# Performance work log

Hardware: AMD Instinct MI355X
Metric: run time of the kernel (lower is better)

The kernel has to match this reference:

```python
import jax, jax.numpy as jnp
import numpy as np

RADIUS = 4
NUM_LEVELS = 4
STRIDES = (1, 1, 1, 1)


def _level_corr(f1, f2, coords, r, stride):
    """Windowed bilinear correlation at one pyramid level.
    f1: [B,C,H,W] (full-res features), f2: [B,C,H2,W2] (level features),
    coords: [B,2,H,W] (x,y) already scaled to f2's resolution.
    Returns [B,(2r+1)^2,H,W].
    """
    B, C, H, W = f1.shape
    H2, W2 = f2.shape[2], f2.shape[3]
    f1t = jnp.transpose(f1, (0, 2, 3, 1))                     # [B,H,W,C]
    f2f = jnp.transpose(f2, (0, 2, 3, 1)).reshape(B, H2 * W2, C)
    d = jnp.arange(-r, r + 1, dtype=f1.dtype) * stride
    dy, dx = jnp.meshgrid(d, d, indexing='ij')
    deltas = jnp.stack([dx.ravel(), dy.ravel()], axis=-1)      # [(2r+1)^2, 2]

    def one_offset(delta):
        x = coords[:, 0] + delta[0]                            # [B,H,W]
        y = coords[:, 1] + delta[1]
        x0 = jnp.floor(x)
        y0 = jnp.floor(y)
        acc = jnp.zeros((B, H, W), f1.dtype)
        # 4 bilinear corners, zero padding outside the feature map
        for cx in (0.0, 1.0):
            for cy in (0.0, 1.0):
                xc = x0 + cx
                yc = y0 + cy
                w = (1.0 - jnp.abs(x - xc)) * (1.0 - jnp.abs(y - yc))
                valid = (xc >= 0) & (xc <= W2 - 1) & (yc >= 0) & (yc <= H2 - 1)
                idx = (jnp.clip(yc, 0, H2 - 1) * W2 + jnp.clip(xc, 0, W2 - 1)).astype(jnp.int32)
                g = jax.vmap(lambda t, i: t[i])(f2f, idx.reshape(B, -1)).reshape(B, H, W, C)
                acc = acc + jnp.where(valid, w, 0.0) * jnp.einsum('bhwc,bhwc->bhw', f1t, g)
        return acc                                             # [B,H,W]

    corr = jax.lax.map(one_offset, deltas)                     # [K,B,H,W]
    return jnp.transpose(corr, (1, 0, 2, 3))                   # [B,K,H,W]


def _corr_block(fmap1, fmap2s, coords):
    C = fmap1.shape[1]
    outs = []
    for i, f2 in enumerate(fmap2s):
        outs.append(_level_corr(fmap1, f2, coords / (2.0 ** i), RADIUS, STRIDES[i]))
    corr = jnp.concatenate(outs, axis=1)                       # [B, L*(2r+1)^2, H, W]
    return corr / jnp.sqrt(jnp.asarray(C, fmap1.dtype))


def setup_inputs() -> dict:
    key = jax.random.key(0)
    ks = jax.random.split(key, 6)
    B, C, H, W = 2, 256, 64, 64
    inp = {'fmap1': jax.random.normal(ks[0], (B, C, H, W), jnp.float32)}
    for i in range(NUM_LEVELS):
        h, w = H >> i, W >> i
        inp['fmap2_%d' % i] = jax.random.normal(ks[1 + i], (B, C, h, w), jnp.float32)
    gy, gx = jnp.meshgrid(jnp.arange(H, dtype=jnp.float32), jnp.arange(W, dtype=jnp.float32), indexing='ij')
    base = jnp.broadcast_to(jnp.stack([gx, gy], 0)[None], (B, 2, H, W))
    flow = 2.0 * jax.random.normal(jax.random.fold_in(key, 99), (B, 2, H, W), jnp.float32)
    inp['coords'] = base + flow
    return inp


def reference(fmap1, fmap2_0, fmap2_1, fmap2_2, fmap2_3, coords):
    return _corr_block(fmap1, [fmap2_0, fmap2_1, fmap2_2, fmap2_3], coords)
```

## Files before the change

### kernel.cpp

```cpp
#include <hip/hip_runtime.h>

#define RADIUS 4
#define KK 81
#define HWP 4096

typedef _Float16 f16x8 __attribute__((ext_vector_type(8)));
typedef _Float16 f16x4 __attribute__((ext_vector_type(4)));
typedef float    f32x4 __attribute__((ext_vector_type(4)));

#define OFF_F1T  0u
#define OFF_L0   4194304u
#define OFF_L1   8388608u
#define OFF_L2   9437184u
#define OFF_L3   9699328u
#define OFF_ZPAD 9764864u
#define OFF_END  9765376u

__global__ __launch_bounds__(256) void stage_kernel(
    const float* __restrict__ f1, const float* __restrict__ l0,
    const float* __restrict__ l1, const float* __restrict__ l2,
    const float* __restrict__ l3, char* __restrict__ wsB)
{
    __shared__ float tile[32][36];
    const int bx = blockIdx.x;
    const int b  = blockIdx.z;
    const int r0 = blockIdx.y * 32;
    const int t  = threadIdx.x;
    if (bx == 0 && blockIdx.y == 0 && b == 0 && t < 128)
        ((float*)(wsB + OFF_ZPAD))[t] = 0.0f;
    const float* src; _Float16* dst; int S, s0i;
    if (bx < 128)      { src = f1; dst = (_Float16*)(wsB + OFF_F1T); S = 4096; s0i = bx; }
    else if (bx < 256) { src = l0; dst = (_Float16*)(wsB + OFF_L0);  S = 4096; s0i = bx - 128; }
    else if (bx < 288) { src = l1; dst = (_Float16*)(wsB + OFF_L1);  S = 1024; s0i = bx - 256; }
    else if (bx < 296) { src = l2; dst = (_Float16*)(wsB + OFF_L2);  S = 256;  s0i = bx - 288; }
    else               { src = l3; dst = (_Float16*)(wsB + OFF_L3);  S = 64;   s0i = bx - 296; }
    const int s0 = s0i * 32;
    src += (size_t)b * 256 * S;
    dst += (size_t)b * S * 256;
    {
        const int row = t >> 3, cg = t & 7;
        *(f32x4*)&tile[row][cg * 4] =
            *(const f32x4*)&src[(size_t)(r0 + row) * S + s0 + cg * 4];
    }
    __syncthreads();
    {
        const int sidx = t >> 3, chg = t & 7;
        f16x4 o;
        o[0] = (_Float16)tile[chg * 4 + 0][sidx];
        o[1] = (_Float16)tile[chg * 4 + 1][sidx];
        o[2] = (_Float16)tile[chg * 4 + 2][sidx];
        o[3] = (_Float16)tile[chg * 4 + 3][sidx];
        *(f16x4*)&dst[(size_t)(s0 + sidx) * 256 + r0 + chg * 4] = o;
    }
}

__global__ __launch_bounds__(256, 2) void corr_mfma_kernel(
    const char* __restrict__ wsB,
    const float* __restrict__ coords,
    float* __restrict__ out)
{
    __shared__ float sD[32][104];
    __shared__ int   sIx[32], sIy[32];
    __shared__ float sW[32][4];
    __shared__ int   sBox[5];

    const int bx   = blockIdx.x;
    const int lvl  = blockIdx.y;
    const int tile = ((bx & 7) << 5) | (bx >> 3);
    const int b    = tile >> 7;
    const int t7   = tile & 127;
    const int tr4  = (t7 >> 3) << 2;
    const int tc8  = (t7 & 7) << 3;
    const int t    = threadIdx.x;
    const int l    = t & 63;
    const int wid  = t >> 6;

    const int sh = 6 - lvl;
    const int W2 = 1 << sh;

    for (int i = t; i < 32 * 104; i += 256)
        ((float*)sD)[i] = 0.0f;

    if (t < 32) {
        const int hwc = ((tr4 + (t >> 3)) << 6) + tc8 + (t & 7);
        const float sc = 1.0f / (float)(1 << lvl);
        const float xs = coords[((size_t)b * 2 + 0) * HWP + hwc] * sc;
        const float ys = coords[((size_t)b * 2 + 1) * HWP + hwc] * sc;
        const float x0f = floorf(xs), y0f = floorf(ys);
        sIx[t] = (int)x0f; sIy[t] = (int)y0f;
        const float fx = xs - x0f, fy = ys - y0f;
        sW[t][0] = (1.f - fx) * (1.f - fy);
        sW[t][1] = fx * (1.f - fy);
        sW[t][2] = (1.f - fx) * fy;
        sW[t][3] = fx * fy;
    }
    __syncthreads();
    if (t == 0) {
        int rlo = 1 << 20, rhi = -(1 << 20), clo = 1 << 20, chi = -(1 << 20);
        for (int px = 0; px < 32; ++px) {
            rlo = min(rlo, sIy[px]); rhi = max(rhi, sIy[px]);
            clo = min(clo, sIx[px]); chi = max(chi, sIx[px]);
        }
        const int rl = max(rlo - RADIUS, 0);
        const int rh = min(rhi + RADIUS + 1, W2 - 1);
        const int cf = max(clo - RADIUS, 0);
        const int ce = min(chi + RADIUS + 1, W2 - 1);
        const int nr = rh - rl + 1;
        const int nt = (ce >= cf) ? ((ce - cf + 16) >> 4) : 0;
        sBox[0] = rl;
        sBox[1] = cf;
        sBox[2] = nt;
        sBox[3] = (nr > 0) ? nr * nt : 0;
        sBox[4] = 65535 / max(nt, 1) + 1;
    }

    const int hwA0 = ((tr4 + ((l & 15) >> 3)) << 6) + tc8 + (l & 7);
    const int hwA1 = ((tr4 + 2 + ((l & 15) >> 3)) << 6) + tc8 + (l & 7);
    const char* ap0 = wsB + OFF_F1T + ((size_t)(b * HWP + hwA0)) * 512 + ((l >> 4) << 4);
    const char* ap1 = wsB + OFF_F1T + ((size_t)(b * HWP + hwA1)) * 512 + ((l >> 4) << 4);
    const f16x8 a00 = __builtin_bit_cast(f16x8, *(const f32x4*)(ap0));
    const f16x8 a01 = __builtin_bit_cast(f16x8, *(const f32x4*)(ap0 + 64));
    const f16x8 a02 = __builtin_bit_cast(f16x8, *(const f32x4*)(ap0 + 128));
    const f16x8 a03 = __builtin_bit_cast(f16x8, *(const f32x4*)(ap0 + 192));
    const f16x8 a04 = __builtin_bit_cast(f16x8, *(const f32x4*)(ap0 + 256));
    const f16x8 a05 = __builtin_bit_cast(f16x8, *(const f32x4*)(ap0 + 320));
    const f16x8 a06 = __builtin_bit_cast(f16x8, *(const f32x4*)(ap0 + 384));
    const f16x8 a07 = __builtin_bit_cast(f16x8, *(const f32x4*)(ap0 + 448));
    const f16x8 a10 = __builtin_bit_cast(f16x8, *(const f32x4*)(ap1));
    const f16x8 a11 = __builtin_bit_cast(f16x8, *(const f32x4*)(ap1 + 64));
    const f16x8 a12 = __builtin_bit_cast(f16x8, *(const f32x4*)(ap1 + 128));
    const f16x8 a13 = __builtin_bit_cast(f16x8, *(const f32x4*)(ap1 + 192));
    const f16x8 a14 = __builtin_bit_cast(f16x8, *(const f32x4*)(ap1 + 256));
    const f16x8 a15 = __builtin_bit_cast(f16x8, *(const f32x4*)(ap1 + 320));
    const f16x8 a16 = __builtin_bit_cast(f16x8, *(const f32x4*)(ap1 + 384));
    const f16x8 a17 = __builtin_bit_cast(f16x8, *(const f32x4*)(ap1 + 448));
    __syncthreads();

    const int rlo = sBox[0], cfi = sBox[1], ntw = sBox[2];
    const int ntot = sBox[3], inv = sBox[4];
    const unsigned lvbase = ((lvl == 0) ? OFF_L0 : (lvl == 1) ? OFF_L1
                           : (lvl == 2) ? OFF_L2 : OFF_L3)
                          + (((unsigned)b << (2 * sh)) << 9);
    const int coff = l & 15;
    const int ksub = (l >> 4) << 4;
    const unsigned zp = OFF_ZPAD + (unsigned)ksub;

    const int pg0 = (l >> 4) << 2;
    const int pg1 = 16 + pg0;
    const int iy0 = sIy[pg0 + 0], ix0 = sIx[pg0 + 0];
    const int iy1 = sIy[pg0 + 1], ix1 = sIx[pg0 + 1];
    const int iy2 = sIy[pg0 + 2], ix2 = sIx[pg0 + 2];
    const int iy3 = sIy[pg0 + 3], ix3 = sIx[pg0 + 3];
    const int iy4 = sIy[pg1 + 0], ix4 = sIx[pg1 + 0];
    const int iy5 = sIy[pg1 + 1], ix5 = sIx[pg1 + 1];
    const int iy6 = sIy[pg1 + 2], ix6 = sIx[pg1 + 2];
    const int iy7 = sIy[pg1 + 3], ix7 = sIx[pg1 + 3];

    asm volatile("s_waitcnt vmcnt(0)" ::: "memory");
    __builtin_amdgcn_sched_barrier(0);

#define DECODE(U_, RR_, JJ_) { const unsigned q__ = ((unsigned)((U_) * inv)) >> 16; \
        JJ_ = (U_) - (int)q__ * ntw; RR_ = rlo + (int)q__; }

#define ISSUE(R_, J_, B0, B1, B2, B3, B4, B5, B6, B7) { \
        const int col_ = cfi + ((J_) << 4) + coff; \
        const bool ok_ = (unsigned)col_ < (unsigned)W2; \
        const unsigned cb_ = ok_ ? (lvbase + ((unsigned)(((R_) << sh) + col_) << 9) + (unsigned)ksub) : zp; \
        const char* gp_ = wsB + cb_; \
        asm volatile("global_load_dwordx4 %0, %1, off"            : "=v"(B0) : "v"(gp_)); \
        asm volatile("global_load_dwordx4 %0, %1, off offset:64"  : "=v"(B1) : "v"(gp_)); \
        asm volatile("global_load_dwordx4 %0, %1, off offset:128" : "=v"(B2) : "v"(gp_)); \
        asm volatile("global_load_dwordx4 %0, %1, off offset:192" : "=v"(B3) : "v"(gp_)); \
        asm volatile("global_load_dwordx4 %0, %1, off offset:256" : "=v"(B4) : "v"(gp_)); \
        asm volatile("global_load_dwordx4 %0, %1, off offset:320" : "=v"(B5) : "v"(gp_)); \
        asm volatile("global_load_dwordx4 %0, %1, off offset:384" : "=v"(B6) : "v"(gp_)); \
        asm volatile("global_load_dwordx4 %0, %1, off offset:448" : "=v"(B7) : "v"(gp_)); }

#define WAITV8 { asm volatile("s_waitcnt vmcnt(8)" ::: "memory"); __builtin_amdgcn_sched_barrier(0); }
#define WAITV0 { asm volatile("s_waitcnt vmcnt(0)" ::: "memory"); __builtin_amdgcn_sched_barrier(0); }

#define CONSUMET(R_, J_, B0, B1, B2, B3, B4, B5, B6, B7) { \
        f32x4 ac00 = {0.f,0.f,0.f,0.f}, ac01 = {0.f,0.f,0.f,0.f}; \
        f32x4 ac10 = {0.f,0.f,0.f,0.f}, ac11 = {0.f,0.f,0.f,0.f}; \
        ac00 = __builtin_amdgcn_mfma_f32_16x16x32_f16(a00, __builtin_bit_cast(f16x8, B0), ac00, 0, 0, 0); \
        ac10 = __builtin_amdgcn_mfma_f32_16x16x32_f16(a10, __builtin_bit_cast(f16x8, B0), ac10, 0, 0, 0); \
        ac01 = __builtin_amdgcn_mfma_f32_16x16x32_f16(a01, __builtin_bit_cast(f16x8, B1), ac01, 0, 0, 0); \
        ac11 = __builtin_amdgcn_mfma_f32_16x16x32_f16(a11, __builtin_bit_cast(f16x8, B1), ac11, 0, 0, 0); \
        ac00 = __builtin_amdgcn_mfma_f32_16x16x32_f16(a02, __builtin_bit_cast(f16x8, B2), ac00, 0, 0, 0); \
        ac10 = __builtin_amdgcn_mfma_f32_16x16x32_f16(a12, __builtin_bit_cast(f16x8, B2), ac10, 0, 0, 0); \
        ac01 = __builtin_amdgcn_mfma_f32_16x16x32_f16(a03, __builtin_bit_cast(f16x8, B3), ac01, 0, 0, 0); \
        ac11 = __builtin_amdgcn_mfma_f32_16x16x32_f16(a13, __builtin_bit_cast(f16x8, B3), ac11, 0, 0, 0); \
        ac00 = __builtin_amdgcn_mfma_f32_16x16x32_f16(a04, __builtin_bit_cast(f16x8, B4), ac00, 0, 0, 0); \
        ac10 = __builtin_amdgcn_mfma_f32_16x16x32_f16(a14, __builtin_bit_cast(f16x8, B4), ac10, 0, 0, 0); \
        ac01 = __builtin_amdgcn_mfma_f32_16x16x32_f16(a05, __builtin_bit_cast(f16x8, B5), ac01, 0, 0, 0); \
        ac11 = __builtin_amdgcn_mfma_f32_16x16x32_f16(a15, __builtin_bit_cast(f16x8, B5), ac11, 0, 0, 0); \
        ac00 = __builtin_amdgcn_mfma_f32_16x16x32_f16(a06, __builtin_bit_cast(f16x8, B6), ac00, 0, 0, 0); \
        ac10 = __builtin_amdgcn_mfma_f32_16x16x32_f16(a16, __builtin_bit_cast(f16x8, B6), ac10, 0, 0, 0); \
        ac01 = __builtin_amdgcn_mfma_f32_16x16x32_f16(a07, __builtin_bit_cast(f16x8, B7), ac01, 0, 0, 0); \
        ac11 = __builtin_amdgcn_mfma_f32_16x16x32_f16(a17, __builtin_bit_cast(f16x8, B7), ac11, 0, 0, 0); \
        const f32x4 s0 = ac00 + ac01; \
        const f32x4 s1 = ac10 + ac11; \
        const int col_ = cfi + ((J_) << 4) + coff; \
        const int p0 = (R_) - iy0 + RADIUS, q0 = col_ - ix0 + RADIUS; \
        if ((unsigned)p0 < 10u && (unsigned)q0 < 10u) sD[pg0 + 0][p0 * 10 + q0] = s0[0]; \
        const int p1 = (R_) - iy1 + RADIUS, q1 = col_ - ix1 + RADIUS; \
        if ((unsigned)p1 < 10u && (unsigned)q1 < 10u) sD[pg0 + 1][p1 * 10 + q1] = s0[1]; \
        const int p2 = (R_) - iy2 + RADIUS, q2 = col_ - ix2 + RADIUS; \
        if ((unsigned)p2 < 10u && (unsigned)q2 < 10u) sD[pg0 + 2][p2 * 10 + q2] = s0[2]; \
        const int p3 = (R_) - iy3 + RADIUS, q3 = col_ - ix3 + RADIUS; \
        if ((unsigned)p3 < 10u && (unsigned)q3 < 10u) sD[pg0 + 3][p3 * 10 + q3] = s0[3]; \
        const int p4 = (R_) - iy4 + RADIUS, q4 = col_ - ix4 + RADIUS; \
        if ((unsigned)p4 < 10u && (unsigned)q4 < 10u) sD[pg1 + 0][p4 * 10 + q4] = s1[0]; \
        const int p5 = (R_) - iy5 + RADIUS, q5 = col_ - ix5 + RADIUS; \
        if ((unsigned)p5 < 10u && (unsigned)q5 < 10u) sD[pg1 + 1][p5 * 10 + q5] = s1[1]; \
        const int p6 = (R_) - iy6 + RADIUS, q6 = col_ - ix6 + RADIUS; \
        if ((unsigned)p6 < 10u && (unsigned)q6 < 10u) sD[pg1 + 2][p6 * 10 + q6] = s1[2]; \
        const int p7 = (R_) - iy7 + RADIUS, q7 = col_ - ix7 + RADIUS; \
        if ((unsigned)p7 < 10u && (unsigned)q7 < 10u) sD[pg1 + 3][p7 * 10 + q7] = s1[3]; }

    {
        f32x4 X0, X1, X2, X3, X4, X5, X6, X7;
        f32x4 Y0, Y1, Y2, Y3, Y4, Y5, Y6, Y7;
        int ua = wid;
        if (ua < ntot) {
            int ra, ja, rb, jb;
            DECODE(ua, ra, ja);
            ISSUE(ra, ja, X0, X1, X2, X3, X4, X5, X6, X7);
            int ub = ua + 4;
            for (;;) {
                const bool bv = (ub < ntot);
                if (bv) { DECODE(ub, rb, jb); ISSUE(rb, jb, Y0, Y1, Y2, Y3, Y4, Y5, Y6, Y7); WAITV8; }
                else    { WAITV0; }
                CONSUMET(ra, ja, X0, X1, X2, X3, X4, X5, X6, X7);
                if (!bv) break;
                ua = ub + 4;
                const bool av = (ua < ntot);
                if (av) { DECODE(ua, ra, ja); ISSUE(ra, ja, X0, X1, X2, X3, X4, X5, X6, X7); WAITV8; }
                else    { WAITV0; }
                CONSUMET(rb, jb, Y0, Y1, Y2, Y3, Y4, Y5, Y6, Y7);
                if (!av) break;
                ub = ua + 4;
            }
        }
    }
#undef DECODE
#undef ISSUE
#undef WAITV8
#undef WAITV0
#undef CONSUMET
    __syncthreads();

    for (int j = t; j < 32 * KK; j += 256) {
        const int px = j & 31;
        const int k  = j >> 5;
        const int p  = (k * 57) >> 9;
        const int q  = k - p * 9;
        const int bi = p * 10 + q;
        const float* dd = sD[px];
        const float v = (sW[px][0] * dd[bi]      + sW[px][1] * dd[bi + 1] +
                         sW[px][2] * dd[bi + 10] + sW[px][3] * dd[bi + 11]) * 0.0625f;
        const int hwp = ((tr4 + (px >> 3)) << 6) + tc8 + (px & 7);
        out[((size_t)b * 324 + lvl * KK + k) * HWP + hwp] = v;
    }
}

__global__ __launch_bounds__(128) void corr_level_kernel(
    const float* __restrict__ f1, const float* __restrict__ f2,
    const float* __restrict__ coords, float* __restrict__ out,
    int H2, int W2, float scale, int lvl)
{
    __shared__ float sf1[256];
    __shared__ float sDl[100];
    const int pix = blockIdx.x;
    const int b   = pix >> 12;
    const int hw  = pix & 4095;
    const int t   = threadIdx.x;
    for (int c = t; c < 256; c += 128)
        sf1[c] = f1[((size_t)b * 256 + c) * 4096 + hw];
    __syncthreads();
    const float xs = coords[((size_t)b * 2 + 0) * 4096 + hw] * scale;
    const float ys = coords[((size_t)b * 2 + 1) * 4096 + hw] * scale;
    const float x0f = floorf(xs), y0f = floorf(ys);
    const float fx = xs - x0f, fy = ys - y0f;
    const int ix0 = (int)x0f, iy0 = (int)y0f;
    if (t < 100) {
        const int p = t / 10, q = t - p * 10;
        const int row = iy0 - 4 + p, col = ix0 - 4 + q;
        float acc = 0.0f;
        if (row >= 0 && row < H2 && col >= 0 && col < W2) {
            const size_t step = (size_t)H2 * W2;
            const size_t base = (size_t)b * 256 * step + (size_t)row * W2 + col;
            #pragma unroll 4
            for (int c = 0; c < 256; ++c)
                acc += f2[base + (size_t)c * step] * sf1[c];
        }
        sDl[t] = acc;
    }
    __syncthreads();
    if (t < 81) {
        const int p = t / 9, q = t - p * 9;
        const float d00 = sDl[p * 10 + q];
        const float d01 = sDl[p * 10 + q + 1];
        const float d10 = sDl[p * 10 + q + 10];
        const float d11 = sDl[p * 10 + q + 11];
        const float v = (1.0f - fy) * ((1.0f - fx) * d00 + fx * d01)
                      + fy * ((1.0f - fx) * d10 + fx * d11);
        out[((size_t)b * 324 + (size_t)lvl * 81 + t) * 4096 + hw] = v * 0.0625f;
    }
}

extern "C" void kernel_launch(void* const* d_in, const int* in_sizes, int n_in,
                              void* d_out, int out_size, void* d_ws, size_t ws_size,
                              hipStream_t stream) {
    (void)out_size;
    const float* f1     = (const float*)d_in[0];
    const float* f2l[4] = {(const float*)d_in[1], (const float*)d_in[2],
                           (const float*)d_in[3], (const float*)d_in[4]};
    const float* coords = (const float*)d_in[5];

    {
        int nbig = 0;
        for (int i = 0; i < n_in; ++i) {
            const int sz = in_sizes[i];
            if (sz == 2097152) {
                if (nbig == 0) f1 = (const float*)d_in[i];
                else           f2l[0] = (const float*)d_in[i];
                ++nbig;
            }
            else if (sz == 524288) f2l[1] = (const float*)d_in[i];
            else if (sz == 131072) f2l[2] = (const float*)d_in[i];
            else if (sz ==  32768) f2l[3] = (const float*)d_in[i];
            else if (sz ==  16384) coords = (const float*)d_in[i];
        }
    }
    float* out = (float*)d_out;
    char*  wsB = (char*)d_ws;

    if (ws_size >= (size_t)OFF_END) {
        stage_kernel<<<dim3(298, 8, 2), dim3(256, 1, 1), 0, stream>>>(
            f1, f2l[0], f2l[1], f2l[2], f2l[3], wsB);
        corr_mfma_kernel<<<dim3(256, 4, 1), 256, 0, stream>>>(wsB, coords, out);
    } else {
        for (int lvl = 0; lvl < 4; ++lvl) {
            const int W2 = 64 >> lvl;
            const float scale = 1.0f / (float)(1 << lvl);
            corr_level_kernel<<<8192, 128, 0, stream>>>(
                f1, f2l[lvl], coords, out, W2, W2, scale, lvl);
        }
    }
}
```

Measured before the change: 45.52 us.

## Enlarge correlation tile to 64 pixels and interleave pyramid levels across blocks

Each block now handles an 8x8 pixel tile (64 query pixels) instead of 4x8, so every loaded level-feature column feeds four MFMA row groups instead of two. This cuts the redundant reloading of overlapping search windows. The grid is flattened to 512 blocks, pairing heavy and light pyramid levels so the work is more balanced. In exchange, LDS use doubles, registers for the A fragments grow (32 f16x8 held live), and the block count halves, which may reduce occupancy and latency hiding.

```diff
diff --git a/kernel.cpp b/kernel.cpp
--- a/kernel.cpp
+++ b/kernel.cpp
@@ -59,30 +59,32 @@
     const float* __restrict__ coords,
     float* __restrict__ out)
 {
-    __shared__ float sD[32][104];
-    __shared__ int   sIx[32], sIy[32];
-    __shared__ float sW[32][4];
+    __shared__ float sD[64][104];
+    __shared__ int   sIx[64], sIy[64];
+    __shared__ float sW[64][4];
     __shared__ int   sBox[5];
 
-    const int bx   = blockIdx.x;
-    const int lvl  = blockIdx.y;
-    const int tile = ((bx & 7) << 5) | (bx >> 3);
-    const int b    = tile >> 7;
-    const int t7   = tile & 127;
-    const int tr4  = (t7 >> 3) << 2;
-    const int tc8  = (t7 & 7) << 3;
-    const int t    = threadIdx.x;
-    const int l    = t & 63;
-    const int wid  = t >> 6;
+    const int id  = blockIdx.x;
+    const int par = id & 1;
+    const int kk  = id >> 1;
+    const int lvl = (par == 0) ? ((kk < 128) ? 0 : 1) : ((kk < 128) ? 3 : 2);
+    const int tid = kk & 127;
+    const int b   = tid >> 6;
+    const int t6  = tid & 63;
+    const int tr8 = (t6 >> 3) << 3;
+    const int tc8 = (t6 & 7) << 3;
+    const int t   = threadIdx.x;
+    const int l   = t & 63;
+    const int wid = t >> 6;
 
     const int sh = 6 - lvl;
     const int W2 = 1 << sh;
 
-    for (int i = t; i < 32 * 104; i += 256)
+    for (int i = t; i < 64 * 104; i += 256)
         ((float*)sD)[i] = 0.0f;
 
-    if (t < 32) {
-        const int hwc = ((tr4 + (t >> 3)) << 6) + tc8 + (t & 7);
+    if (t < 64) {
+        const int hwc = ((tr8 + (t >> 3)) << 6) + tc8 + (t & 7);
         const float sc = 1.0f / (float)(1 << lvl);
         const float xs = coords[((size_t)b * 2 + 0) * HWP + hwc] * sc;
         const float ys = coords[((size_t)b * 2 + 1) * HWP + hwc] * sc;
@@ -97,7 +99,7 @@
     __syncthreads();
     if (t == 0) {
         int rlo = 1 << 20, rhi = -(1 << 20), clo = 1 << 20, chi = -(1 << 20);
-        for (int px = 0; px < 32; ++px) {
+        for (int px = 0; px < 64; ++px) {
             rlo = min(rlo, sIy[px]); rhi = max(rhi, sIy[px]);
             clo = min(clo, sIx[px]); chi = max(chi, sIx[px]);
         }
@@ -114,26 +116,28 @@
         sBox[4] = 65535 / max(nt, 1) + 1;
     }
 
-    const int hwA0 = ((tr4 + ((l & 15) >> 3)) << 6) + tc8 + (l & 7);
-    const int hwA1 = ((tr4 + 2 + ((l & 15) >> 3)) << 6) + tc8 + (l & 7);
-    const char* ap0 = wsB + OFF_F1T + ((size_t)(b * HWP + hwA0)) * 512 + ((l >> 4) << 4);
-    const char* ap1 = wsB + OFF_F1T + ((size_t)(b * HWP + hwA1)) * 512 + ((l >> 4) << 4);
-    const f16x8 a00 = __builtin_bit_cast(f16x8, *(const f32x4*)(ap0));
-    const f16x8 a01 = __builtin_bit_cast(f16x8, *(const f32x4*)(ap0 + 64));
-    const f16x8 a02 = __builtin_bit_cast(f16x8, *(const f32x4*)(ap0 + 128));
-    const f16x8 a03 = __builtin_bit_cast(f16x8, *(const f32x4*)(ap0 + 192));
-    const f16x8 a04 = __builtin_bit_cast(f16x8, *(const f32x4*)(ap0 + 256));
-    const f16x8 a05 = __builtin_bit_cast(f16x8, *(const f32x4*)(ap0 + 320));
-    const f16x8 a06 = __builtin_bit_cast(f16x8, *(const f32x4*)(ap0 + 384));
-    const f16x8 a07 = __builtin_bit_cast(f16x8, *(const f32x4*)(ap0 + 448));
-    const f16x8 a10 = __builtin_bit_cast(f16x8, *(const f32x4*)(ap1));
-    const f16x8 a11 = __builtin_bit_cast(f16x8, *(const f32x4*)(ap1 + 64));
-    const f16x8 a12 = __builtin_bit_cast(f16x8, *(const f32x4*)(ap1 + 128));
-    const f16x8 a13 = __builtin_bit_cast(f16x8, *(const f32x4*)(ap1 + 192));
-    const f16x8 a14 = __builtin_bit_cast(f16x8, *(const f32x4*)(ap1 + 256));
-    const f16x8 a15 = __builtin_bit_cast(f16x8, *(const f32x4*)(ap1 + 320));
-    const f16x8 a16 = __builtin_bit_cast(f16x8, *(const f32x4*)(ap1 + 384));
-    const f16x8 a17 = __builtin_bit_cast(f16x8, *(const f32x4*)(ap1 + 448));
+#define ALOADS(S_) \
+    const int hwA##S_ = ((tr8 + 2 * (S_) + ((l & 15) >> 3)) << 6) + tc8 + (l & 7); \
+    const char* ap##S_ = wsB + OFF_F1T + ((size_t)(b * HWP + hwA##S_)) * 512 + ((l >> 4) << 4); \
+    const f16x8 a##S_##0 = __builtin_bit_cast(f16x8, *(const f32x4*)(ap##S_)); \
+    const f16x8 a##S_##1 = __builtin_bit_cast(f16x8, *(const f32x4*)(ap##S_ + 64)); \
+    const f16x8 a##S_##2 = __builtin_bit_cast(f16x8, *(const f32x4*)(ap##S_ + 128)); \
+    const f16x8 a##S_##3 = __builtin_bit_cast(f16x8, *(const f32x4*)(ap##S_ + 192)); \
+    const f16x8 a##S_##4 = __builtin_bit_cast(f16x8, *(const f32x4*)(ap##S_ + 256)); \
+    const f16x8 a##S_##5 = __builtin_bit_cast(f16x8, *(const f32x4*)(ap##S_ + 320)); \
+    const f16x8 a##S_##6 = __builtin_bit_cast(f16x8, *(const f32x4*)(ap##S_ + 384)); \
+    const f16x8 a##S_##7 = __builtin_bit_cast(f16x8, *(const f32x4*)(ap##S_ + 448));
+    ALOADS(0) ALOADS(1) ALOADS(2) ALOADS(3)
+#undef ALOADS
+
+    const int pgl = (l >> 4) << 2;
+#define PKD(S_, J_) const int pk##S_##J_ = \
+        ((4 - sIy[(S_) * 16 + pgl + (J_)]) << 16) | ((4 - sIx[(S_) * 16 + pgl + (J_)]) & 0xffff);
+    PKD(0,0) PKD(0,1) PKD(0,2) PKD(0,3)
+    PKD(1,0) PKD(1,1) PKD(1,2) PKD(1,3)
+    PKD(2,0) PKD(2,1) PKD(2,2) PKD(2,3)
+    PKD(3,0) PKD(3,1) PKD(3,2) PKD(3,3)
+#undef PKD
     __syncthreads();
 
     const int rlo = sBox[0], cfi = sBox[1], ntw = sBox[2];
@@ -144,17 +148,6 @@
     const int coff = l & 15;
     const int ksub = (l >> 4) << 4;
     const unsigned zp = OFF_ZPAD + (unsigned)ksub;
-
-    const int pg0 = (l >> 4) << 2;
-    const int pg1 = 16 + pg0;
-    const int iy0 = sIy[pg0 + 0], ix0 = sIx[pg0 + 0];
-    const int iy1 = sIy[pg0 + 1], ix1 = sIx[pg0 + 1];
-    const int iy2 = sIy[pg0 + 2], ix2 = sIx[pg0 + 2];
-    const int iy3 = sIy[pg0 + 3], ix3 = sIx[pg0 + 3];
-    const int iy4 = sIy[pg1 + 0], ix4 = sIx[pg1 + 0];
-    const int iy5 = sIy[pg1 + 1], ix5 = sIx[pg1 + 1];
-    const int iy6 = sIy[pg1 + 2], ix6 = sIx[pg1 + 2];
-    const int iy7 = sIy[pg1 + 3], ix7 = sIx[pg1 + 3];
 
     asm volatile("s_waitcnt vmcnt(0)" ::: "memory");
     __builtin_amdgcn_sched_barrier(0);
@@ -179,44 +172,33 @@
 #define WAITV8 { asm volatile("s_waitcnt vmcnt(8)" ::: "memory"); __builtin_amdgcn_sched_barrier(0); }
 #define WAITV0 { asm volatile("s_waitcnt vmcnt(0)" ::: "memory"); __builtin_amdgcn_sched_barrier(0); }
 
+#define CONSET(S_, B0, B1, B2, B3, B4, B5, B6, B7) { \
+        f32x4 ac0 = {0.f,0.f,0.f,0.f}, ac1 = {0.f,0.f,0.f,0.f}; \
+        ac0 = __builtin_amdgcn_mfma_f32_16x16x32_f16(a##S_##0, __builtin_bit_cast(f16x8, B0), ac0, 0, 0, 0); \
+        ac1 = __builtin_amdgcn_mfma_f32_16x16x32_f16(a##S_##1, __builtin_bit_cast(f16x8, B1), ac1, 0, 0, 0); \
+        ac0 = __builtin_amdgcn_mfma_f32_16x16x32_f16(a##S_##2, __builtin_bit_cast(f16x8, B2), ac0, 0, 0, 0); \
+        ac1 = __builtin_amdgcn_mfma_f32_16x16x32_f16(a##S_##3, __builtin_bit_cast(f16x8, B3), ac1, 0, 0, 0); \
+        ac0 = __builtin_amdgcn_mfma_f32_16x16x32_f16(a##S_##4, __builtin_bit_cast(f16x8, B4), ac0, 0, 0, 0); \
+        ac1 = __builtin_amdgcn_mfma_f32_16x16x32_f16(a##S_##5, __builtin_bit_cast(f16x8, B5), ac1, 0, 0, 0); \
+        ac0 = __builtin_amdgcn_mfma_f32_16x16x32_f16(a##S_##6, __builtin_bit_cast(f16x8, B6), ac0, 0, 0, 0); \
+        ac1 = __builtin_amdgcn_mfma_f32_16x16x32_f16(a##S_##7, __builtin_bit_cast(f16x8, B7), ac1, 0, 0, 0); \
+        const f32x4 ss = ac0 + ac1; \
+        { const int p = row_ + (pk##S_##0 >> 16), q = col_ + ((pk##S_##0 << 16) >> 16); \
+          if ((unsigned)p < 10u && (unsigned)q < 10u) sD[(S_)*16 + pgl + 0][p * 10 + q] = ss[0]; } \
+        { const int p = row_ + (pk##S_##1 >> 16), q = col_ + ((pk##S_##1 << 16) >> 16); \
+          if ((unsigned)p < 10u && (unsigned)q < 10u) sD[(S_)*16 + pgl + 1][p * 10 + q] = ss[1]; } \
+        { const int p = row_ + (pk##S_##2 >> 16), q = col_ + ((pk##S_##2 << 16) >> 16); \
+          if ((unsigned)p < 10u && (unsigned)q < 10u) sD[(S_)*16 + pgl + 2][p * 10 + q] = ss[2]; } \
+        { const int p = row_ + (pk##S_##3 >> 16), q = col_ + ((pk##S_##3 << 16) >> 16); \
+          if ((unsigned)p < 10u && (unsigned)q < 10u) sD[(S_)*16 + pgl + 3][p * 10 + q] = ss[3]; } }
+
 #define CONSUMET(R_, J_, B0, B1, B2, B3, B4, B5, B6, B7) { \
-        f32x4 ac00 = {0.f,0.f,0.f,0.f}, ac01 = {0.f,0.f,0.f,0.f}; \
-        f32x4 ac10 = {0.f,0.f,0.f,0.f}, ac11 = {0.f,0.f,0.f,0.f}; \
-        ac00 = __builtin_amdgcn_mfma_f32_16x16x32_f16(a00, __builtin_bit_cast(f16x8, B0), ac00, 0, 0, 0); \
-        ac10 = __builtin_amdgcn_mfma_f32_16x16x32_f16(a10, __builtin_bit_cast(f16x8, B0), ac10, 0, 0, 0); \
-        ac01 = __builtin_amdgcn_mfma_f32_16x16x32_f16(a01, __builtin_bit_cast(f16x8, B1), ac01, 0, 0, 0); \
-        ac11 = __builtin_amdgcn_mfma_f32_16x16x32_f16(a11, __builtin_bit_cast(f16x8, B1), ac11, 0, 0, 0); \
-        ac00 = __builtin_amdgcn_mfma_f32_16x16x32_f16(a02, __builtin_bit_cast(f16x8, B2), ac00, 0, 0, 0); \
-        ac10 = __builtin_amdgcn_mfma_f32_16x16x32_f16(a12, __builtin_bit_cast(f16x8, B2), ac10, 0, 0, 0); \
-        ac01 = __builtin_amdgcn_mfma_f32_16x16x32_f16(a03, __builtin_bit_cast(f16x8, B3), ac01, 0, 0, 0); \
-        ac11 = __builtin_amdgcn_mfma_f32_16x16x32_f16(a13, __builtin_bit_cast(f16x8, B3), ac11, 0, 0, 0); \
-        ac00 = __builtin_amdgcn_mfma_f32_16x16x32_f16(a04, __builtin_bit_cast(f16x8, B4), ac00, 0, 0, 0); \
-        ac10 = __builtin_amdgcn_mfma_f32_16x16x32_f16(a14, __builtin_bit_cast(f16x8, B4), ac10, 0, 0, 0); \
-        ac01 = __builtin_amdgcn_mfma_f32_16x16x32_f16(a05, __builtin_bit_cast(f16x8, B5), ac01, 0, 0, 0); \
-        ac11 = __builtin_amdgcn_mfma_f32_16x16x32_f16(a15, __builtin_bit_cast(f16x8, B5), ac11, 0, 0, 0); \
-        ac00 = __builtin_amdgcn_mfma_f32_16x16x32_f16(a06, __builtin_bit_cast(f16x8, B6), ac00, 0, 0, 0); \
-        ac10 = __builtin_amdgcn_mfma_f32_16x16x32_f16(a16, __builtin_bit_cast(f16x8, B6), ac10, 0, 0, 0); \
-        ac01 = __builtin_amdgcn_mfma_f32_16x16x32_f16(a07, __builtin_bit_cast(f16x8, B7), ac01, 0, 0, 0); \
-        ac11 = __builtin_amdgcn_mfma_f32_16x16x32_f16(a17, __builtin_bit_cast(f16x8, B7), ac11, 0, 0, 0); \
-        const f32x4 s0 = ac00 + ac01; \
-        const f32x4 s1 = ac10 + ac11; \
+        const int row_ = (R_); \
         const int col_ = cfi + ((J_) << 4) + coff; \
-        const int p0 = (R_) - iy0 + RADIUS, q0 = col_ - ix0 + RADIUS; \
-        if ((unsigned)p0 < 10u && (unsigned)q0 < 10u) sD[pg0 + 0][p0 * 10 + q0] = s0[0]; \
-        const int p1 = (R_) - iy1 + RADIUS, q1 = col_ - ix1 + RADIUS; \
-        if ((unsigned)p1 < 10u && (unsigned)q1 < 10u) sD[pg0 + 1][p1 * 10 + q1] = s0[1]; \
-        const int p2 = (R_) - iy2 + RADIUS, q2 = col_ - ix2 + RADIUS; \
-        if ((unsigned)p2 < 10u && (unsigned)q2 < 10u) sD[pg0 + 2][p2 * 10 + q2] = s0[2]; \
-        const int p3 = (R_) - iy3 + RADIUS, q3 = col_ - ix3 + RADIUS; \
-        if ((unsigned)p3 < 10u && (unsigned)q3 < 10u) sD[pg0 + 3][p3 * 10 + q3] = s0[3]; \
-        const int p4 = (R_) - iy4 + RADIUS, q4 = col_ - ix4 + RADIUS; \
-        if ((unsigned)p4 < 10u && (unsigned)q4 < 10u) sD[pg1 + 0][p4 * 10 + q4] = s1[0]; \
-        const int p5 = (R_) - iy5 + RADIUS, q5 = col_ - ix5 + RADIUS; \
-        if ((unsigned)p5 < 10u && (unsigned)q5 < 10u) sD[pg1 + 1][p5 * 10 + q5] = s1[1]; \
-        const int p6 = (R_) - iy6 + RADIUS, q6 = col_ - ix6 + RADIUS; \
-        if ((unsigned)p6 < 10u && (unsigned)q6 < 10u) sD[pg1 + 2][p6 * 10 + q6] = s1[2]; \
-        const int p7 = (R_) - iy7 + RADIUS, q7 = col_ - ix7 + RADIUS; \
-        if ((unsigned)p7 < 10u && (unsigned)q7 < 10u) sD[pg1 + 3][p7 * 10 + q7] = s1[3]; }
+        CONSET(0, B0, B1, B2, B3, B4, B5, B6, B7) \
+        CONSET(1, B0, B1, B2, B3, B4, B5, B6, B7) \
+        CONSET(2, B0, B1, B2, B3, B4, B5, B6, B7) \
+        CONSET(3, B0, B1, B2, B3, B4, B5, B6, B7) }
 
     {
         f32x4 X0, X1, X2, X3, X4, X5, X6, X7;
@@ -247,19 +229,20 @@
 #undef ISSUE
 #undef WAITV8
 #undef WAITV0
+#undef CONSET
 #undef CONSUMET
     __syncthreads();
 
-    for (int j = t; j < 32 * KK; j += 256) {
-        const int px = j & 31;
-        const int k  = j >> 5;
+    for (int j = t; j < 64 * KK; j += 256) {
+        const int px = j & 63;
+        const int k  = j >> 6;
         const int p  = (k * 57) >> 9;
         const int q  = k - p * 9;
         const int bi = p * 10 + q;
         const float* dd = sD[px];
         const float v = (sW[px][0] * dd[bi]      + sW[px][1] * dd[bi + 1] +
                          sW[px][2] * dd[bi + 10] + sW[px][3] * dd[bi + 11]) * 0.0625f;
-        const int hwp = ((tr4 + (px >> 3)) << 6) + tc8 + (px & 7);
+        const int hwp = ((tr8 + (px >> 3)) << 6) + tc8 + (px & 7);
         out[((size_t)b * 324 + lvl * KK + k) * HWP + hwp] = v;
     }
 }
@@ -339,7 +322,7 @@
     if (ws_size >= (size_t)OFF_END) {
         stage_kernel<<<dim3(298, 8, 2), dim3(256, 1, 1), 0, stream>>>(
             f1, f2l[0], f2l[1], f2l[2], f2l[3], wsB);
-        corr_mfma_kernel<<<dim3(256, 4, 1), 256, 0, stream>>>(wsB, coords, out);
+        corr_mfma_kernel<<<dim3(512, 1, 1), 256, 0, stream>>>(wsB, coords, out);
     } else {
         for (int lvl = 0; lvl < 4; ++lvl) {
             const int W2 = 64 >> lvl;
```

Result: slower. 54.30 us (+19.3%).
